# Kernel optimization log

Hardware: AMD Instinct MI355X
Metric: run time of the kernel (lower is better)

The kernel has to match this reference:

```python
import math
import jax, jax.numpy as jnp
import numpy as np

C = 1024  # n_embd
B, T = 4, 2048
H = 4 * C  # mlp hidden
EPS = 1e-5


def setup_inputs() -> dict:
    key = jax.random.key(0)
    ks = jax.random.split(key, 8)
    s = 0.02
    return {
        "x": jax.random.normal(ks[0], (B, T, C), jnp.float32),
        "ln1_g": jnp.ones((C,), jnp.float32),
        "ln1_b": jnp.zeros((C,), jnp.float32),
        "w_attn": jax.random.normal(ks[1], (C, 3 * C), jnp.float32) * s,
        "b_attn": jnp.zeros((3 * C,), jnp.float32),
        "w_proj": jax.random.normal(ks[2], (C, C), jnp.float32) * s,
        "b_proj": jnp.zeros((C,), jnp.float32),
        "ln2_g": jnp.ones((C,), jnp.float32),
        "ln2_b": jnp.zeros((C,), jnp.float32),
        "w_fc": jax.random.normal(ks[3], (C, H), jnp.float32) * s,
        "b_fc": jnp.zeros((H,), jnp.float32),
        "w_mlp_proj": jax.random.normal(ks[4], (H, C), jnp.float32) * s,
        "b_mlp_proj": jnp.zeros((C,), jnp.float32),
    }


def _layernorm(x, g, b):
    mu = jnp.mean(x, axis=-1, keepdims=True)
    var = jnp.mean(jnp.square(x - mu), axis=-1, keepdims=True)
    return (x - mu) * jax.lax.rsqrt(var + EPS) * g + b


def _new_gelu(x):
    c = math.sqrt(2.0 / math.pi)
    return 0.5 * x * (1.0 + jnp.tanh(c * (x + 0.044715 * x * x * x)))


def reference(x, ln1_g, ln1_b, w_attn, b_attn, w_proj, b_proj,
              ln2_g, ln2_b, w_fc, b_fc, w_mlp_proj, b_mlp_proj):
    # --- attention sublayer (single-head, full-dim, no causal mask) ---
    h = _layernorm(x, ln1_g, ln1_b)
    qkv = h @ w_attn + b_attn              # [B,T,3C]
    q, k, v = jnp.split(qkv, 3, axis=-1)   # each [B,T,C]
    scale = 1.0 / math.sqrt(C)
    att = jnp.einsum("btc,bsc->bts", q, k) * scale  # [B,T,T]
    att = jax.nn.softmax(att, axis=-1)
    y = jnp.einsum("bts,bsc->btc", att, v)
    y = y @ w_proj + b_proj
    x = x + y
    # --- MLP sublayer ---
    h2 = _layernorm(x, ln2_g, ln2_b)
    m = _new_gelu(h2 @ w_fc + b_fc) @ w_mlp_proj + b_mlp_proj
    return x + m
```

## Files before the change

### kernel.cpp

```cpp
#include <hip/hip_runtime.h>

typedef __bf16 bf16;
typedef bf16 bf16x8 __attribute__((ext_vector_type(8)));
typedef bf16 bf16x4 __attribute__((ext_vector_type(4)));
typedef float f32x4 __attribute__((ext_vector_type(4)));

#define C_DIM 1024
#define T_DIM 2048
#define B_DIM 4
#define H_DIM 4096

__device__ inline void gld_lds16(const bf16* g, bf16* l) {
    __builtin_amdgcn_global_load_lds(
        (const __attribute__((address_space(1))) unsigned int*)g,
        (__attribute__((address_space(3))) unsigned int*)l,
        16, 0, 0);
}

__device__ inline float fast_gelu(float u) {
    float k2 = 1.5957691216057308f * u + 0.07135480895843475f * u * u * u;
    float t = __expf(-k2);
    return u * __builtin_amdgcn_rcpf(1.0f + t);
}

template <int EPI, typename OutT, int BN>
__launch_bounds__(512, 2)
__global__ void gemm8p(const bf16* __restrict__ A, int lda, long long sA,
                       const bf16* __restrict__ Bt, int ldb, long long sB,
                       OutT* __restrict__ Cout, int ldc, long long sC,
                       const float* __restrict__ bias,
                       const float* __restrict__ resid, long long sR,
                       float alpha, int K) {
    constexpr int BQ = BN / 128;
    constexpr int FM = (BN == 256) ? 8 : 4;
    constexpr int AW = (BN == 256) ? 128 : 64;

    const int z = blockIdx.z;
    A += (long long)z * sA;
    Bt += (long long)z * sB;
    Cout += (long long)z * sC;
    if (resid) resid += (long long)z * sR;

    const int rowBase = blockIdx.x * 256;
    const int colBase = blockIdx.y * BN;

    __shared__ __align__(16) bf16 As[2 * 2 * 256 * 32];
    __shared__ __align__(16) bf16 Bs[2 * 2 * BN * 32];

    const int tid = threadIdx.x;
    const int w = tid >> 6;
    const int lane = tid & 63;
    const int wm = (BN == 256) ? (w >> 2) : (w >> 1);
    const int wn = (BN == 256) ? (w & 3) : (w & 1);
    const int lr = lane & 15, lc = lane >> 4;

    const int gchunk = (tid & 3) ^ ((tid >> 3) & 3);
    const bf16* Ag = A + (size_t)(rowBase + (tid >> 2)) * lda + gchunk * 8;
    const bf16* Bg = Bt + (size_t)(colBase + (tid >> 2)) * ldb + gchunk * 8;
    const size_t ldaL = (size_t)lda, ldbL = (size_t)ldb;
    bf16* AsW = As + w * 512;
    bf16* BsW = Bs + w * 512;

    const int rchunk = lc ^ ((lr >> 1) & 3);
    const int aBase = wm * (AW * 32) + lr * 32 + rchunk * 8;
    const int bBase = wn * 2048 + lr * 32 + rchunk * 8;

#define STAGE_A(buf, ks, tau) do {                                         \
        const bf16* _g = Ag + (size_t)(tau) * 64 + (ks) * 32;              \
        bf16* _l = AsW + ((buf) * 2 + (ks)) * 8192;                        \
        gld_lds16(_g, _l);                                                 \
        gld_lds16(_g + 128 * ldaL, _l + 4096);                             \
    } while (0)

#define STAGE_B(buf, ks, tau) do {                                         \
        const bf16* _g = Bg + (size_t)(tau) * 64 + (ks) * 32;              \
        bf16* _l = BsW + ((buf) * 2 + (ks)) * (BN * 32);                   \
        gld_lds16(_g, _l);                                                 \
        if constexpr (BQ == 2) gld_lds16(_g + 128 * ldbL, _l + 4096);      \
    } while (0)

#define LOAD_AF(buf, ks) do {                                              \
        _Pragma("unroll")                                                  \
        for (int i = 0; i < FM; i++)                                       \
            af[i] = *(const bf16x8*)(As + aBase + ((buf) * 2 + (ks)) * 8192 \
                                     + i * 512);                           \
    } while (0)

#define LOAD_BF(buf, ks) do {                                              \
        _Pragma("unroll")                                                  \
        for (int j = 0; j < 4; j++)                                        \
            bfv[j] = *(const bf16x8*)(Bs + bBase + ((buf) * 2 + (ks)) * (BN * 32) \
                                      + j * 512);                          \
    } while (0)

#define MMAALL() do {                                                      \
        __builtin_amdgcn_s_setprio(1);                                     \
        _Pragma("unroll")                                                  \
        for (int i = 0; i < FM; i++)                                       \
            _Pragma("unroll")                                              \
            for (int j = 0; j < 4; j++)                                    \
                acc[i][j] = __builtin_amdgcn_mfma_f32_16x16x32_bf16(       \
                    af[i], bfv[j], acc[i][j], 0, 0, 0);                    \
        __builtin_amdgcn_s_setprio(0);                                     \
    } while (0)

#define BAR() __builtin_amdgcn_s_barrier()
#define VMCS() do {                                                        \
        if constexpr (BN == 256) asm volatile("s_waitcnt vmcnt(8)" ::: "memory"); \
        else                     asm volatile("s_waitcnt vmcnt(6)" ::: "memory"); \
    } while (0)
#define VMCH() do {                                                        \
        if constexpr (BN == 256) asm volatile("s_waitcnt vmcnt(4)" ::: "memory"); \
        else                     asm volatile("s_waitcnt vmcnt(3)" ::: "memory"); \
    } while (0)
#define VMC0() asm volatile("s_waitcnt vmcnt(0)" ::: "memory")

    f32x4 acc[FM][4] = {};
    bf16x8 af[FM], bfv[4];

    const int NT = K >> 6;

    STAGE_A(0, 0, 0); STAGE_B(0, 0, 0);
    STAGE_A(0, 1, 0); STAGE_B(0, 1, 0);
    STAGE_A(1, 0, 1); STAGE_B(1, 0, 1);
    BAR();

    for (int t = 0; t < NT - 2; t += 2) {
        VMCS();
        LOAD_AF(0, 0); LOAD_BF(0, 0);
        STAGE_A(1, 1, t + 1); STAGE_B(1, 1, t + 1);
        BAR(); MMAALL(); BAR();

        VMCS();
        LOAD_AF(0, 1); LOAD_BF(0, 1);
        STAGE_A(0, 0, t + 2); STAGE_B(0, 0, t + 2);
        BAR(); MMAALL(); BAR();

        VMCS();
        LOAD_AF(1, 0); LOAD_BF(1, 0);
        STAGE_A(0, 1, t + 2); STAGE_B(0, 1, t + 2);
        BAR(); MMAALL(); BAR();

        VMCS();
        LOAD_AF(1, 1); LOAD_BF(1, 1);
        STAGE_A(1, 0, t + 3); STAGE_B(1, 0, t + 3);
        BAR(); MMAALL(); BAR();
    }

    VMCS();
    LOAD_AF(0, 0); LOAD_BF(0, 0);
    STAGE_A(1, 1, NT - 1); STAGE_B(1, 1, NT - 1);
    BAR(); MMAALL(); BAR();

    VMCS();
    LOAD_AF(0, 1); LOAD_BF(0, 1);
    BAR(); MMAALL(); BAR();

    VMCH();
    LOAD_AF(1, 0); LOAD_BF(1, 0);
    BAR(); MMAALL(); BAR();

    VMC0();
    LOAD_AF(1, 1); LOAD_BF(1, 1);
    MMAALL();

#undef STAGE_A
#undef STAGE_B
#undef LOAD_AF
#undef LOAD_BF
#undef MMAALL
#undef BAR
#undef VMCS
#undef VMCH
#undef VMC0

    float bval[4];
#pragma unroll
    for (int j = 0; j < 4; j++)
        bval[j] = bias ? bias[colBase + wn * 64 + j * 16 + lr] : 0.0f;

#pragma unroll
    for (int fi = 0; fi < FM; fi++) {
        const int row = rowBase + wm * AW + fi * 16 + lc * 4;
#pragma unroll
        for (int fj = 0; fj < 4; fj++) {
            const int col = colBase + wn * 64 + fj * 16 + lr;
#pragma unroll
            for (int r = 0; r < 4; r++) {
                float v = acc[fi][fj][r] * alpha + bval[fj];
                if constexpr (EPI == 1) v = fast_gelu(v);
                if constexpr (EPI == 2) v += resid[(size_t)(row + r) * ldc + col];
                Cout[(size_t)(row + r) * ldc + col] = (OutT)v;
            }
        }
    }
}

__launch_bounds__(256)
__global__ void ln_kernel(const float* __restrict__ x, const float* __restrict__ g,
                          const float* __restrict__ b, bf16* __restrict__ out) {
    __shared__ float red[4];
    const int row = blockIdx.x;
    const int tid = threadIdx.x;
    const float4* xr = (const float4*)(x + (size_t)row * C_DIM);
    float4 v = xr[tid];
    float s = v.x + v.y + v.z + v.w;
#pragma unroll
    for (int m = 32; m; m >>= 1) s += __shfl_xor(s, m, 64);
    if ((tid & 63) == 0) red[tid >> 6] = s;
    __syncthreads();
    const float mu = (red[0] + red[1] + red[2] + red[3]) * (1.0f / C_DIM);
    const float dx = v.x - mu, dy = v.y - mu, dz = v.z - mu, dw = v.w - mu;
    float q = dx * dx + dy * dy + dz * dz + dw * dw;
#pragma unroll
    for (int m = 32; m; m >>= 1) q += __shfl_xor(q, m, 64);
    __syncthreads();
    if ((tid & 63) == 0) red[tid >> 6] = q;
    __syncthreads();
    const float var = (red[0] + red[1] + red[2] + red[3]) * (1.0f / C_DIM);
    const float rs = rsqrtf(var + 1e-5f);
    const float4 gg = ((const float4*)g)[tid];
    const float4 bb = ((const float4*)b)[tid];
    bf16x4 o;
    o[0] = (bf16)(dx * rs * gg.x + bb.x);
    o[1] = (bf16)(dy * rs * gg.y + bb.y);
    o[2] = (bf16)(dz * rs * gg.z + bb.z);
    o[3] = (bf16)(dw * rs * gg.w + bb.w);
    ((bf16x4*)(out + (size_t)row * C_DIM))[tid] = o;
}

__launch_bounds__(256)
__global__ void softmax_kernel(const bf16* __restrict__ S, bf16* __restrict__ P) {
    __shared__ float red[4];
    const size_t base = (size_t)blockIdx.x * T_DIM;
    const int tid = threadIdx.x;
    bf16x8 sv = ((const bf16x8*)(S + base))[tid];
    float e[8];
#pragma unroll
    for (int i = 0; i < 8; i++) e[i] = (float)sv[i];
    float mx = e[0];
#pragma unroll
    for (int i = 1; i < 8; i++) mx = fmaxf(mx, e[i]);
#pragma unroll
    for (int m = 32; m; m >>= 1) mx = fmaxf(mx, __shfl_xor(mx, m, 64));
    if ((tid & 63) == 0) red[tid >> 6] = mx;
    __syncthreads();
    mx = fmaxf(fmaxf(red[0], red[1]), fmaxf(red[2], red[3]));
    float s = 0.0f;
#pragma unroll
    for (int i = 0; i < 8; i++) {
        e[i] = __expf(e[i] - mx);
        s += e[i];
    }
#pragma unroll
    for (int m = 32; m; m >>= 1) s += __shfl_xor(s, m, 64);
    __syncthreads();
    if ((tid & 63) == 0) red[tid >> 6] = s;
    __syncthreads();
    const float inv = 1.0f / (red[0] + red[1] + red[2] + red[3]);
    bf16x8 p;
#pragma unroll
    for (int i = 0; i < 8; i++) p[i] = (bf16)(e[i] * inv);
    ((bf16x8*)(P + base))[tid] = p;
}

__global__ void transpose_f2b_all(const float* __restrict__ s0, bf16* __restrict__ d0,
                                  const float* __restrict__ s1, bf16* __restrict__ d1,
                                  const float* __restrict__ s2, bf16* __restrict__ d2,
                                  const float* __restrict__ s3, bf16* __restrict__ d3) {
    __shared__ float tile[32][33];
    int id = blockIdx.x;
    const float* src;
    bf16* dst;
    int R, Cc, local;
    if (id < 3072)       { src = s0; dst = d0; R = 1024; Cc = 3072; local = id; }
    else if (id < 4096)  { src = s1; dst = d1; R = 1024; Cc = 1024; local = id - 3072; }
    else if (id < 8192)  { src = s2; dst = d2; R = 1024; Cc = 4096; local = id - 4096; }
    else                 { src = s3; dst = d3; R = 4096; Cc = 1024; local = id - 8192; }
    const int tilesX = Cc >> 5;
    const int bx = (local % tilesX) * 32;
    const int by = (local / tilesX) * 32;
    const int tx = threadIdx.x, ty = threadIdx.y;
    for (int i = ty; i < 32; i += 8)
        tile[i][tx] = src[(size_t)(by + i) * Cc + bx + tx];
    __syncthreads();
    for (int i = ty; i < 32; i += 8)
        dst[(size_t)(bx + i) * R + by + tx] = (bf16)tile[tx][i];
}

__global__ void transpose_b2b(const bf16* __restrict__ src, int ldsrc, long long sstride,
                              bf16* __restrict__ dst, long long dstride, int R) {
    __shared__ bf16 tile[32][33];
    src += (long long)blockIdx.z * sstride;
    dst += (long long)blockIdx.z * dstride;
    const int bx = blockIdx.x * 32;
    const int by = blockIdx.y * 32;
    const int tx = threadIdx.x, ty = threadIdx.y;
    for (int i = ty; i < 32; i += 8)
        tile[i][tx] = src[(size_t)(by + i) * ldsrc + bx + tx];
    __syncthreads();
    for (int i = ty; i < 32; i += 8)
        dst[(size_t)(bx + i) * R + by + tx] = tile[tx][i];
}

extern "C" void kernel_launch(void* const* d_in, const int* in_sizes, int n_in,
                              void* d_out, int out_size, void* d_ws, size_t ws_size,
                              hipStream_t stream) {
    const float* x      = (const float*)d_in[0];
    const float* ln1_g  = (const float*)d_in[1];
    const float* ln1_b  = (const float*)d_in[2];
    const float* w_attn = (const float*)d_in[3];
    const float* b_attn = (const float*)d_in[4];
    const float* w_proj = (const float*)d_in[5];
    const float* b_proj = (const float*)d_in[6];
    const float* ln2_g  = (const float*)d_in[7];
    const float* ln2_b  = (const float*)d_in[8];
    const float* w_fc   = (const float*)d_in[9];
    const float* b_fc   = (const float*)d_in[10];
    const float* w_mlp  = (const float*)d_in[11];
    const float* b_mlp  = (const float*)d_in[12];
    float* out = (float*)d_out;

    const int M = B_DIM * T_DIM;

    char* base = (char*)d_ws;
    size_t off = 0;
    auto alloc = [&](size_t bytes) -> char* {
        char* p = base + off;
        off += (bytes + 255) & ~(size_t)255;
        return p;
    };
    bf16* wT_attn = (bf16*)alloc((size_t)3072 * 1024 * 2);
    bf16* wT_proj = (bf16*)alloc((size_t)1024 * 1024 * 2);
    bf16* wT_fc   = (bf16*)alloc((size_t)4096 * 1024 * 2);
    bf16* wT_mlp  = (bf16*)alloc((size_t)1024 * 4096 * 2);
    bf16* h       = (bf16*)alloc((size_t)M * 1024 * 2);
    bf16* qkv     = (bf16*)alloc((size_t)M * 3072 * 2);
    bf16* vT      = (bf16*)alloc((size_t)B_DIM * 1024 * 2048 * 2);
    bf16* S       = (bf16*)alloc((size_t)B_DIM * 2048 * 2048 * 2);
    bf16* P       = (bf16*)alloc((size_t)B_DIM * 2048 * 2048 * 2);
    bf16* y       = (bf16*)alloc((size_t)M * 1024 * 2);
    float* x2     = (float*)alloc((size_t)M * 1024 * 4);
    bf16* act     = (bf16*)S;

    const dim3 tb(32, 8);

    transpose_f2b_all<<<12288, tb, 0, stream>>>(w_attn, wT_attn, w_proj, wT_proj,
                                                w_fc, wT_fc, w_mlp, wT_mlp);

    ln_kernel<<<M, 256, 0, stream>>>(x, ln1_g, ln1_b, h);

    gemm8p<0, bf16, 128><<<dim3(32, 24, 1), 512, 0, stream>>>(
        h, 1024, 0, wT_attn, 1024, 0, qkv, 3072, 0, b_attn, nullptr, 0, 1.0f, 1024);

    transpose_b2b<<<dim3(1024 / 32, 2048 / 32, B_DIM), tb, 0, stream>>>(
        qkv + 2 * C_DIM, 3072, (long long)T_DIM * 3072, vT, (long long)C_DIM * T_DIM, T_DIM);

    gemm8p<0, bf16, 256><<<dim3(8, 8, B_DIM), 512, 0, stream>>>(
        qkv, 3072, (long long)T_DIM * 3072,
        qkv + C_DIM, 3072, (long long)T_DIM * 3072,
        S, 2048, (long long)T_DIM * T_DIM, nullptr, nullptr, 0, 0.03125f, 1024);

    softmax_kernel<<<B_DIM * T_DIM, 256, 0, stream>>>(S, P);

    gemm8p<0, bf16, 128><<<dim3(8, 8, B_DIM), 512, 0, stream>>>(
        P, 2048, (long long)T_DIM * T_DIM,
        vT, 2048, (long long)C_DIM * T_DIM,
        y, 1024, (long long)T_DIM * C_DIM, nullptr, nullptr, 0, 1.0f, 2048);

    gemm8p<2, float, 128><<<dim3(32, 8, 1), 512, 0, stream>>>(
        y, 1024, 0, wT_proj, 1024, 0, x2, 1024, 0, b_proj, x, 0, 1.0f, 1024);

    ln_kernel<<<M, 256, 0, stream>>>(x2, ln2_g, ln2_b, h);

    gemm8p<1, bf16, 256><<<dim3(32, 16, 1), 512, 0, stream>>>(
        h, 1024, 0, wT_fc, 1024, 0, act, 4096, 0, b_fc, nullptr, 0, 1.0f, 1024);

    gemm8p<2, float, 128><<<dim3(32, 8, 1), 512, 0, stream>>>(
        act, 4096, 0, wT_mlp, 4096, 0, out, 1024, 0, b_mlp, x2, 0, 1.0f, 4096);
}
```

Baseline: 519.0 us.

## Restructure GEMM mainloop into 4-slot ring with register double-buffered fragments

Replaces the 2x2 LDS buffer schedule with a four-slot ring of 32-wide K slices, prefetching three slices ahead. Fragments are double-buffered in registers (af0/af1, bv0/bv1) so LDS reads for the next slice overlap the current MFMA batch. sched_barrier keeps the compiler from reordering around the waits. The aim is to hide LDS and global latency behind MFMA work, at the cost of more vector registers and possible occupancy or spill risk.

```diff
diff --git a/kernel.cpp b/kernel.cpp
--- a/kernel.cpp
+++ b/kernel.cpp
@@ -44,8 +44,8 @@
     const int rowBase = blockIdx.x * 256;
     const int colBase = blockIdx.y * BN;
 
-    __shared__ __align__(16) bf16 As[2 * 2 * 256 * 32];
-    __shared__ __align__(16) bf16 Bs[2 * 2 * BN * 32];
+    __shared__ __align__(16) bf16 As[4 * 256 * 32];
+    __shared__ __align__(16) bf16 Bs[4 * BN * 32];
 
     const int tid = threadIdx.x;
     const int w = tid >> 6;
@@ -65,113 +65,104 @@
     const int aBase = wm * (AW * 32) + lr * 32 + rchunk * 8;
     const int bBase = wn * 2048 + lr * 32 + rchunk * 8;
 
-#define STAGE_A(buf, ks, tau) do {                                         \
-        const bf16* _g = Ag + (size_t)(tau) * 64 + (ks) * 32;              \
-        bf16* _l = AsW + ((buf) * 2 + (ks)) * 8192;                        \
-        gld_lds16(_g, _l);                                                 \
-        gld_lds16(_g + 128 * ldaL, _l + 4096);                             \
+#define STAGE(slot, tau) do {                                              \
+        const bf16* _ga = Ag + (size_t)(tau) * 32;                         \
+        bf16* _la = AsW + (slot) * 8192;                                   \
+        gld_lds16(_ga, _la);                                               \
+        gld_lds16(_ga + 128 * ldaL, _la + 4096);                           \
+        const bf16* _gb = Bg + (size_t)(tau) * 32;                         \
+        bf16* _lb = BsW + (slot) * (BN * 32);                              \
+        gld_lds16(_gb, _lb);                                               \
+        if constexpr (BQ == 2) gld_lds16(_gb + 128 * ldbL, _lb + 4096);    \
     } while (0)
 
-#define STAGE_B(buf, ks, tau) do {                                         \
-        const bf16* _g = Bg + (size_t)(tau) * 64 + (ks) * 32;              \
-        bf16* _l = BsW + ((buf) * 2 + (ks)) * (BN * 32);                   \
-        gld_lds16(_g, _l);                                                 \
-        if constexpr (BQ == 2) gld_lds16(_g + 128 * ldbL, _l + 4096);      \
-    } while (0)
-
-#define LOAD_AF(buf, ks) do {                                              \
+#define LOAD_AB(afd, bvd, slot) do {                                       \
         _Pragma("unroll")                                                  \
         for (int i = 0; i < FM; i++)                                       \
-            af[i] = *(const bf16x8*)(As + aBase + ((buf) * 2 + (ks)) * 8192 \
-                                     + i * 512);                           \
-    } while (0)
-
-#define LOAD_BF(buf, ks) do {                                              \
+            afd[i] = *(const bf16x8*)(As + aBase + (slot) * 8192 + i * 512); \
         _Pragma("unroll")                                                  \
         for (int j = 0; j < 4; j++)                                        \
-            bfv[j] = *(const bf16x8*)(Bs + bBase + ((buf) * 2 + (ks)) * (BN * 32) \
-                                      + j * 512);                          \
+            bvd[j] = *(const bf16x8*)(Bs + bBase + (slot) * (BN * 32) + j * 512); \
     } while (0)
 
-#define MMAALL() do {                                                      \
+#define MMA(afs, bvs) do {                                                 \
         __builtin_amdgcn_s_setprio(1);                                     \
         _Pragma("unroll")                                                  \
         for (int i = 0; i < FM; i++)                                       \
             _Pragma("unroll")                                              \
             for (int j = 0; j < 4; j++)                                    \
                 acc[i][j] = __builtin_amdgcn_mfma_f32_16x16x32_bf16(       \
-                    af[i], bfv[j], acc[i][j], 0, 0, 0);                    \
+                    afs[i], bvs[j], acc[i][j], 0, 0, 0);                   \
         __builtin_amdgcn_s_setprio(0);                                     \
     } while (0)
 
+#define SB() __builtin_amdgcn_sched_barrier(0)
 #define BAR() __builtin_amdgcn_s_barrier()
-#define VMCS() do {                                                        \
-        if constexpr (BN == 256) asm volatile("s_waitcnt vmcnt(8)" ::: "memory"); \
-        else                     asm volatile("s_waitcnt vmcnt(6)" ::: "memory"); \
-    } while (0)
-#define VMCH() do {                                                        \
+#define VMCG() do {                                                        \
         if constexpr (BN == 256) asm volatile("s_waitcnt vmcnt(4)" ::: "memory"); \
         else                     asm volatile("s_waitcnt vmcnt(3)" ::: "memory"); \
     } while (0)
 #define VMC0() asm volatile("s_waitcnt vmcnt(0)" ::: "memory")
 
     f32x4 acc[FM][4] = {};
-    bf16x8 af[FM], bfv[4];
-
-    const int NT = K >> 6;
-
-    STAGE_A(0, 0, 0); STAGE_B(0, 0, 0);
-    STAGE_A(0, 1, 0); STAGE_B(0, 1, 0);
-    STAGE_A(1, 0, 1); STAGE_B(1, 0, 1);
+    bf16x8 af0[FM], af1[FM], bv0[4], bv1[4];
+
+    const int NP = K >> 5;
+
+    STAGE(0, 0);
+    STAGE(1, 1);
+    STAGE(2, 2);
+    VMCG();
     BAR();
-
-    for (int t = 0; t < NT - 2; t += 2) {
-        VMCS();
-        LOAD_AF(0, 0); LOAD_BF(0, 0);
-        STAGE_A(1, 1, t + 1); STAGE_B(1, 1, t + 1);
-        BAR(); MMAALL(); BAR();
-
-        VMCS();
-        LOAD_AF(0, 1); LOAD_BF(0, 1);
-        STAGE_A(0, 0, t + 2); STAGE_B(0, 0, t + 2);
-        BAR(); MMAALL(); BAR();
-
-        VMCS();
-        LOAD_AF(1, 0); LOAD_BF(1, 0);
-        STAGE_A(0, 1, t + 2); STAGE_B(0, 1, t + 2);
-        BAR(); MMAALL(); BAR();
-
-        VMCS();
-        LOAD_AF(1, 1); LOAD_BF(1, 1);
-        STAGE_A(1, 0, t + 3); STAGE_B(1, 0, t + 3);
-        BAR(); MMAALL(); BAR();
+    LOAD_AB(af0, bv0, 0);
+
+    for (int kt = 0; kt < NP - 4; kt += 4) {
+        LOAD_AB(af1, bv1, 1);
+        STAGE(3, kt + 3);
+        SB(); BAR();
+        MMA(af0, bv0);
+        VMCG(); BAR();
+        LOAD_AB(af0, bv0, 2);
+        STAGE(0, kt + 4);
+        SB(); BAR();
+        MMA(af1, bv1);
+        VMCG(); BAR();
+        LOAD_AB(af1, bv1, 3);
+        STAGE(1, kt + 5);
+        SB(); BAR();
+        MMA(af0, bv0);
+        VMCG(); BAR();
+        LOAD_AB(af0, bv0, 0);
+        STAGE(2, kt + 6);
+        SB(); BAR();
+        MMA(af1, bv1);
+        VMCG(); BAR();
     }
 
-    VMCS();
-    LOAD_AF(0, 0); LOAD_BF(0, 0);
-    STAGE_A(1, 1, NT - 1); STAGE_B(1, 1, NT - 1);
-    BAR(); MMAALL(); BAR();
-
-    VMCS();
-    LOAD_AF(0, 1); LOAD_BF(0, 1);
-    BAR(); MMAALL(); BAR();
-
-    VMCH();
-    LOAD_AF(1, 0); LOAD_BF(1, 0);
-    BAR(); MMAALL(); BAR();
-
-    VMC0();
-    LOAD_AF(1, 1); LOAD_BF(1, 1);
-    MMAALL();
-
-#undef STAGE_A
-#undef STAGE_B
-#undef LOAD_AF
-#undef LOAD_BF
-#undef MMAALL
+    LOAD_AB(af1, bv1, 1);
+    STAGE(3, NP - 1);
+    SB(); BAR();
+    MMA(af0, bv0);
+    VMCG(); BAR();
+
+    LOAD_AB(af0, bv0, 2);
+    SB(); BAR();
+    MMA(af1, bv1);
+    VMC0(); BAR();
+
+    LOAD_AB(af1, bv1, 3);
+    SB(); BAR();
+    MMA(af0, bv0);
+    BAR();
+
+    MMA(af1, bv1);
+
+#undef STAGE
+#undef LOAD_AB
+#undef MMA
+#undef SB
 #undef BAR
-#undef VMCS
-#undef VMCH
+#undef VMCG
 #undef VMC0
 
     float bval[4];
```

New measurement: 564.9 us. 8.9% more time.
